# Kernel tuning notes

Hardware: AMD Instinct MI355X
Metric: run time of the kernel (lower is better)

The kernel has to match this reference:

```python
import jax, jax.numpy as jnp
import numpy as np

NEG_SLOPE_GAT = 0.2    # PyG GATConv default negative_slope
NEG_SLOPE_ACT = 0.01   # F.leaky_relu default
D_DIRECTIONS = 4       # len(target): message directions per variable (uniform in this setup)
GAT_HEADS = 4


def gru_cell(x, h, Wih, Whh, bih, bhh):
    # torch.nn.GRUCell math; Wih [3H, in], Whh [3H, H]
    gi = x @ Wih.T + bih
    gh = h @ Whh.T + bhh
    ir, iz, inn = jnp.split(gi, 3, axis=1)
    hr, hz, hn = jnp.split(gh, 3, axis=1)
    r = jax.nn.sigmoid(ir + hr)
    z = jax.nn.sigmoid(iz + hz)
    n = jnp.tanh(inn + r * hn)
    return (1.0 - z) * n + z * h


def gat_conv(x, W, a_src, a_dst, bias, src, dst, heads, concat):
    # PyG GATConv (self-loops already included in src/dst)
    N = x.shape[0]
    C = W.shape[1] // heads
    h = (x @ W).reshape(N, heads, C)
    as_ = jnp.einsum('nhc,hc->nh', h, a_src)
    ad = jnp.einsum('nhc,hc->nh', h, a_dst)
    e = jax.nn.leaky_relu(as_[src] + ad[dst], NEG_SLOPE_GAT)  # [E, heads]
    m = jax.ops.segment_max(e, dst, num_segments=N)
    ex = jnp.exp(e - m[dst])
    den = jax.ops.segment_sum(ex, dst, num_segments=N)
    alpha = ex / den[dst]
    out = jax.ops.segment_sum(h[src] * alpha[:, :, None], dst, num_segments=N)
    if concat:
        return out.reshape(N, heads * C) + bias
    return out.mean(axis=1) + bias


def setup_inputs():
    key = jax.random.key(0)
    ki = iter(jax.random.split(key, 64))
    nk = lambda: next(ki)
    Nx, A, B = 100000, 50000, 50000
    IC, PD = 16, 3
    GH = IC - PD  # gru hidden = 13
    E, M, G, L, H, OC = 2000000, 1024, 1024, 4, 4, 32
    Ntot = Nx + A + B

    def p(*shape):
        return jax.random.normal(nk(), shape, jnp.float32) * 0.05

    inp = {}
    inp['x'] = jax.random.normal(nk(), (Nx, IC), jnp.float32)
    inp['edge_index'] = jax.random.randint(nk(), (2, E), 0, Ntot)
    inp['ass_to_sum_msg'] = jax.random.normal(nk(), (A, 1), jnp.float32)
    inp['ass_to_sum_hidden'] = jax.random.normal(nk(), (A, GH), jnp.float32)
    inp['sum_to_ass_msg'] = jax.random.normal(nk(), (B, 1), jnp.float32)
    inp['sum_to_ass_hidden'] = jax.random.normal(nk(), (B, GH), jnp.float32)
    inp['prefix'] = jax.random.normal(nk(), (A + B, PD), jnp.float32)
    inp['function_node_idxes'] = jax.random.randint(nk(), (M,), 0, Ntot)
    # regularized neighbor_idx_info: group g has direction idx=group_idx[g], src list group_src[g]
    # with idx at position 0 (out_i == 0) and no other entry equal to idx.
    gidx = jax.random.randint(nk(), (G,), 0, M)
    gs = jax.random.randint(nk(), (G, L), 0, M)
    rest = jnp.where(gs[:, 1:] == gidx[:, None], (gidx[:, None] + 1) % M, gs[:, 1:])
    inp['group_idx'] = gidx
    inp['group_src'] = jnp.concatenate([gidx[:, None], rest], axis=1)
    # GRU params
    for g in ('gru1', 'gru2'):
        inp[g + '_Wih'] = p(3 * GH, 1)
        inp[g + '_Whh'] = p(3 * GH, GH)
        inp[g + '_bih'] = p(3 * GH)
        inp[g + '_bhh'] = p(3 * GH)
    # GATConv params (W stored [in, heads*out], used as x @ W)
    inp['W1'] = p(IC, 32); inp['asrc1'] = p(4, 8); inp['adst1'] = p(4, 8); inp['b1'] = p(32)
    inp['W2'] = p(32, 32); inp['asrc2'] = p(4, 8); inp['adst2'] = p(4, 8); inp['b2'] = p(32)
    inp['W3'] = p(32, 32); inp['asrc3'] = p(4, 8); inp['adst3'] = p(4, 8); inp['b3'] = p(32)
    inp['W4'] = p(32, 4 * OC); inp['asrc4'] = p(4, OC); inp['adst4'] = p(4, OC); inp['b4'] = p(OC)
    # Attention heads: Wq/Wk [H, OC, OC] (applied as v @ Wq[h]), Ws [H, 2*OC], bs [H]
    inp['Wq'] = p(H, OC, OC); inp['Wk'] = p(H, OC, OC); inp['Ws'] = p(H, 2 * OC); inp['bs'] = p(H)
    return inp


def reference(x, edge_index, ass_to_sum_msg, ass_to_sum_hidden, sum_to_ass_msg,
              sum_to_ass_hidden, prefix, function_node_idxes, group_idx, group_src,
              gru1_Wih, gru1_Whh, gru1_bih, gru1_bhh,
              gru2_Wih, gru2_Whh, gru2_bih, gru2_bhh,
              W1, asrc1, adst1, b1, W2, asrc2, adst2, b2,
              W3, asrc3, adst3, b3, W4, asrc4, adst4, b4,
              Wq, Wk, Ws, bs):
    h1 = gru_cell(ass_to_sum_msg, ass_to_sum_hidden, gru1_Wih, gru1_Whh, gru1_bih, gru1_bhh)
    h2 = gru_cell(sum_to_ass_msg, sum_to_ass_hidden, gru2_Wih, gru2_Whh, gru2_bih, gru2_bhh)
    hidden = jnp.concatenate([h1, h2], axis=0)
    hidden = jnp.concatenate([prefix, hidden], axis=1)
    xx = jnp.concatenate([x, hidden], axis=0)
    N = xx.shape[0]
    loop = jnp.arange(N)
    src = jnp.concatenate([edge_index[0], loop])  # add self loops (PyG default)
    dst = jnp.concatenate([edge_index[1], loop])
    xx = jax.nn.leaky_relu(gat_conv(xx, W1, asrc1, adst1, b1, src, dst, GAT_HEADS, True), NEG_SLOPE_ACT)
    xx = jax.nn.leaky_relu(gat_conv(xx, W2, asrc2, adst2, b2, src, dst, GAT_HEADS, True), NEG_SLOPE_ACT)
    xx = jax.nn.leaky_relu(gat_conv(xx, W3, asrc3, adst3, b3, src, dst, GAT_HEADS, True), NEG_SLOPE_ACT)
    xx = jax.nn.leaky_relu(gat_conv(xx, W4, asrc4, adst4, b4, src, dst, GAT_HEADS, False), NEG_SLOPE_ACT)
    pooling = xx[function_node_idxes]  # [M, OC]
    hdim = pooling.shape[1]
    # score(i,j,h) = sigmoid((pooling_i @ Wq_h) . ws_q_h + (pooling_j @ Wk_h) . ws_k_h + bs_h)
    # (associativity: equals sigmoid(score_proj(cat([q_proj, k_proj]))) of the original)
    Vq = jnp.einsum('hdo,ho->hd', Wq, Ws[:, :hdim])
    Vk = jnp.einsum('hdo,ho->hd', Wk, Ws[:, hdim:])
    sq = pooling @ Vq.T  # [M, H]
    sk = pooling @ Vk.T  # [M, H]
    scores = jax.nn.sigmoid(sq[:, None, :] + sk[None, :, :] + bs)  # [M, M, H]; flat n -> (n//M, n%M)
    idx = group_idx
    nbr = group_src[:, 1:]  # idx itself sits at position 0 and is removed
    gathered = scores[idx[:, None], nbr]  # [G, L-1, H]
    trg = scores[idx, idx]                # [G, H]
    score_sum = gathered.mean(axis=1)
    tw = jax.nn.softmax(jnp.stack([score_sum, trg], axis=0), axis=0)  # [2, G, H]
    w = jax.nn.softmax(gathered, axis=1) * tw[0][:, None, :] * (D_DIRECTIONS - 1)
    weights = jnp.concatenate([tw[1][:, None, :], w], axis=1)  # [G, L, H] (out_i == 0)
    return weights, h1, h2
```

## Files before the change

kernel.cpp:

```cpp
#include <hip/hip_runtime.h>
#include <hip/hip_bf16.h>

#define NXD   100000
#define AROWS 50000
#define NND   200000
#define EED   2000000
#define ETOT  2200000
#define GHD   13
#define MMD   1024

#define OUT_H1 16384
#define OUT_H2 (16384 + AROWS * GHD)

#define NB    196
#define BSH   10
#define CAP   16000
#define TILE  4096

#define ASM_BLK    7422
#define GRU_BLK    392
#define FEAT_BLK   1563

typedef __hip_bfloat16 bf16;
typedef unsigned int uvec4 __attribute__((ext_vector_type(4)));

__device__ __forceinline__ float bf2f(bf16 v) { return __bfloat162float(v); }
__device__ __forceinline__ float sigm(float x) { return 1.f / (1.f + __expf(-x)); }
__device__ __forceinline__ float tanhfast(float x) {
    x = fminf(15.f, fmaxf(-15.f, x));
    float t = __expf(-2.f * x);
    return (1.f - t) / (1.f + t);
}
__device__ __forceinline__ float lrelu(float x, float s) { return x > 0.f ? x : s * x; }

__device__ __forceinline__ unsigned short f2bf_bits(float v) {
    bf16 b = __float2bfloat16(v);
    return *reinterpret_cast<unsigned short*>(&b);
}
__device__ __forceinline__ float bflo(unsigned int u) { return __uint_as_float((u & 0xFFFFu) << 16); }
__device__ __forceinline__ float bfhi(unsigned int u) { return __uint_as_float(u & 0xFFFF0000u); }

__device__ __forceinline__ float loadF(const void* p, size_t i, int f32) {
    return f32 ? ((const float*)p)[i] : bf2f(((const bf16*)p)[i]);
}
__device__ __forceinline__ void storeF(void* p, size_t i, float v, int f32) {
    if (f32) ((float*)p)[i] = v;
    else ((bf16*)p)[i] = __float2bfloat16(v);
}

__device__ __forceinline__ int flag_from_x(const void* xp, int tid, int* fl) {
    if (tid < 64) {
        const unsigned short* u = (const unsigned short*)xp;
        unsigned short b = u[tid * 2];
        int e = (b >> 7) & 0xFF;
        int viol = (e == 0xFF) || (e < 64) || (e > 190);
        unsigned long long mask = __ballot(viol != 0);
        if (tid == 0) *fl = (__popcll(mask) > 8) ? 1 : 0;
    }
    __syncthreads();
    return *fl;
}

__global__ void bin_kernel(const int* __restrict__ src_e, const int* __restrict__ dst_e,
                           int* __restrict__ gtail, unsigned int* __restrict__ stage) {
    __shared__ int hist[NB];
    __shared__ int base[NB];
    __shared__ int cur[NB];
    int tid = threadIdx.x;
    for (int i = tid; i < NB; i += 256) hist[i] = 0;
    __syncthreads();
    int t0 = blockIdx.x * TILE;
    int tend = t0 + TILE; if (tend > ETOT) tend = ETOT;
    for (int t = t0 + tid; t < tend; t += 256) {
        int d = (t < EED) ? dst_e[t] : (t - EED);
        atomicAdd(&hist[d >> BSH], 1);
    }
    __syncthreads();
    for (int i = tid; i < NB; i += 256) {
        int c = hist[i];
        base[i] = (c > 0) ? atomicAdd(&gtail[i], c) : 0;
        cur[i] = 0;
    }
    __syncthreads();
    for (int t = t0 + tid; t < tend; t += 256) {
        int s, d;
        if (t < EED) { s = src_e[t]; d = dst_e[t]; } else { s = d = t - EED; }
        int b = d >> BSH;
        int p = base[b] + atomicAdd(&cur[b], 1);
        if (p < CAP)
            stage[(size_t)b * CAP + p] = ((unsigned int)(d & 1023) << 18) | (unsigned int)s;
    }
}

__global__ void asmgru_kernel(const void* __restrict__ x, const void* __restrict__ prefix,
                              const void* __restrict__ msg1, const void* __restrict__ hid1,
                              const void* __restrict__ Wih1, const void* __restrict__ Whh1,
                              const void* __restrict__ bih1, const void* __restrict__ bhh1,
                              const void* __restrict__ msg2, const void* __restrict__ hid2,
                              const void* __restrict__ Wih2, const void* __restrict__ Whh2,
                              const void* __restrict__ bih2, const void* __restrict__ bhh2,
                              void* __restrict__ dout, bf16* __restrict__ bufA) {
    __shared__ float WhhL[39 * 13], WihL[39], bihL[39], bhhL[39];
    __shared__ int fl;
    int bid = blockIdx.x, tid = threadIdx.x;
    int f = flag_from_x(x, tid, &fl);
    if (bid < ASM_BLK) {
        int t = bid * 256 + tid;
        if (t < NXD * 16) {
            bufA[t] = __float2bfloat16(loadF(x, t, f));
        } else {
            int u = t - NXD * 16;
            if (u < NXD * 3) {
                int r = u / 3, c = u - r * 3;
                bufA[(size_t)(NXD + r) * 16 + c] = __float2bfloat16(loadF(prefix, u, f));
            }
        }
        return;
    }
    int vb = bid - ASM_BLK;
    int which = vb >= 196;
    const void* msg = which ? msg2 : msg1;
    const void* hid = which ? hid2 : hid1;
    const void* Wih = which ? Wih2 : Wih1;
    const void* Whh = which ? Whh2 : Whh1;
    const void* bih = which ? bih2 : bih1;
    const void* bhh = which ? bhh2 : bhh1;
    size_t houtbase = which ? (size_t)OUT_H2 : (size_t)OUT_H1;
    int rowbase = which ? AROWS : 0;
    int blk = vb - (which ? 196 : 0);
    for (int i = tid; i < 39 * 13; i += 256) WhhL[i] = loadF(Whh, i, f);
    if (tid < 39) { WihL[tid] = loadF(Wih, tid, f); bihL[tid] = loadF(bih, tid, f); bhhL[tid] = loadF(bhh, tid, f); }
    __syncthreads();
    int n = blk * 256 + tid;
    if (n >= AROWS) return;
    float xv = loadF(msg, n, f);
    float h[GHD];
#pragma unroll
    for (int k = 0; k < GHD; k++) h[k] = loadF(hid, n * GHD + k, f);
#pragma unroll
    for (int k = 0; k < GHD; k++) {
        float gir = fmaf(xv, WihL[k],      bihL[k]);
        float giz = fmaf(xv, WihL[13 + k], bihL[13 + k]);
        float gin = fmaf(xv, WihL[26 + k], bihL[26 + k]);
        float ghr = bhhL[k], ghz = bhhL[13 + k], ghn = bhhL[26 + k];
#pragma unroll
        for (int q = 0; q < GHD; q++) {
            ghr = fmaf(h[q], WhhL[k * 13 + q],        ghr);
            ghz = fmaf(h[q], WhhL[(13 + k) * 13 + q], ghz);
            ghn = fmaf(h[q], WhhL[(26 + k) * 13 + q], ghn);
        }
        float r = sigm(gir + ghr);
        float z = sigm(giz + ghz);
        float nn = tanhfast(gin + r * ghn);
        float o = (1.f - z) * nn + z * h[k];
        storeF(dout, houtbase + (size_t)n * GHD + k, o, f);
        bufA[(size_t)(NXD + rowbase + n) * 16 + 3 + k] = __float2bfloat16(o);
    }
}

template <int K>
__device__ __forceinline__ void feat_body(const bf16* __restrict__ xx,
                                          const void* __restrict__ W,
                                          bf16* __restrict__ hbuf, int f,
                                          int vbid, int tid) {
    int j = tid & 31;
    float Wc[K];
#pragma unroll
    for (int k = 0; k < K; k++) Wc[k] = loadF(W, k * 32 + j, f);
    int half = vbid * 8 + (tid >> 5);
    if (half >= NND / 16) return;
    int n0 = half * 16;
#pragma unroll 4
    for (int n = n0; n < n0 + 16; n++) {
        const uvec4* xr4 = (const uvec4*)(xx + (size_t)n * K);
        float v = 0.f;
#pragma unroll
        for (int q = 0; q < K / 8; q++) {
            uvec4 u = xr4[q];
            v = fmaf(bflo(u.x), Wc[q * 8 + 0], v);
            v = fmaf(bfhi(u.x), Wc[q * 8 + 1], v);
            v = fmaf(bflo(u.y), Wc[q * 8 + 2], v);
            v = fmaf(bfhi(u.y), Wc[q * 8 + 3], v);
            v = fmaf(bflo(u.z), Wc[q * 8 + 4], v);
            v = fmaf(bfhi(u.z), Wc[q * 8 + 5], v);
            v = fmaf(bflo(u.w), Wc[q * 8 + 6], v);
            v = fmaf(bfhi(u.w), Wc[q * 8 + 7], v);
        }
        hbuf[(size_t)n * 32 + j] = __float2bfloat16(v);
    }
}

__global__ void mid_kernel(const unsigned int* __restrict__ stage, const int* __restrict__ gtail,
                           int* __restrict__ offs, int* __restrict__ csr,
                           const bf16* __restrict__ xx, const void* __restrict__ W,
                           bf16* __restrict__ hbuf, const void* __restrict__ x) {
    __shared__ int cnt[1024];
    __shared__ int loc[1024];
    __shared__ int cur[1024];
    __shared__ int lds[256];
    __shared__ int fl;
    int bid = blockIdx.x, tid = threadIdx.x;
    if (bid >= NB) {
        int f = flag_from_x(x, tid, &fl);
        feat_body<16>(xx, W, hbuf, f, bid - NB, tid);
        return;
    }
    int b = bid;
    int v = (tid < NB) ? gtail[tid] : 0;
    lds[tid] = v; __syncthreads();
    for (int off = 1; off < 256; off <<= 1) {
        int t2 = (tid >= off) ? lds[tid - off] : 0;
        __syncthreads();
        lds[tid] += t2;
        __syncthreads();
    }
    __shared__ int ebs;
    if (tid == b) ebs = lds[tid] - v;
    __syncthreads();
    int eb = ebs;
    int nE = gtail[b]; if (nE > CAP) nE = CAP;
    const unsigned int* st = stage + (size_t)b * CAP;
    for (int i = tid; i < 1024; i += 256) cnt[i] = 0;
    __syncthreads();
    for (int i = tid; i < nE; i += 256)
        atomicAdd(&cnt[st[i] >> 18], 1);
    __syncthreads();
    int c0 = cnt[tid * 4], c1 = cnt[tid * 4 + 1], c2 = cnt[tid * 4 + 2], c3 = cnt[tid * 4 + 3];
    int s = c0 + c1 + c2 + c3;
    lds[tid] = s; __syncthreads();
    for (int off = 1; off < 256; off <<= 1) {
        int t2 = (tid >= off) ? lds[tid - off] : 0;
        __syncthreads();
        lds[tid] += t2;
        __syncthreads();
    }
    int run = lds[tid] - s;
    loc[tid * 4]     = run;
    loc[tid * 4 + 1] = run + c0;
    loc[tid * 4 + 2] = run + c0 + c1;
    loc[tid * 4 + 3] = run + c0 + c1 + c2;
    __syncthreads();
    int nodebase = b << BSH;
    for (int i = tid; i < 1024; i += 256) {
        cur[i] = loc[i];
        int n = nodebase + i;
        if (n < NND) offs[n] = eb + loc[i];
    }
    if (b == 0 && tid == 0) offs[NND] = ETOT;
    __syncthreads();
    for (int i = tid; i < nE; i += 256) {
        unsigned int e = st[i];
        int dl = e >> 18;
        int src = e & 0x3FFFF;
        int p = atomicAdd(&cur[dl], 1);
        csr[eb + p] = src;
    }
}

template <int K>
__global__ void feat_kernel(const bf16* __restrict__ xx, const void* __restrict__ W,
                            bf16* __restrict__ hbuf, const void* __restrict__ x) {
    __shared__ int fl;
    int tid = threadIdx.x;
    int f = flag_from_x(x, tid, &fl);
    feat_body<K>(xx, W, hbuf, f, blockIdx.x, tid);
}

__global__ void __launch_bounds__(256, 8)
agg_kernel(const bf16* __restrict__ hbuf, const int* __restrict__ offs,
           const int* __restrict__ csr, const void* __restrict__ asrc,
           const void* __restrict__ adst, const void* __restrict__ bias,
           bf16* __restrict__ xxout, const void* __restrict__ x) {
    __shared__ float bl[32], asl[32], adl[32];
    __shared__ int fl;
    int tid = threadIdx.x;
    int f = flag_from_x(x, tid, &fl);
    if (tid < 32) {
        bl[tid]  = loadF(bias, tid, f);
        asl[tid] = loadF(asrc, tid, f);
        adl[tid] = loadF(adst, tid, f);
    }
    __syncthreads();
    int n = blockIdx.x * 64 + (tid >> 2);
    int j = tid & 3;
    int cb = 8 * j;
    float A0 = asl[cb], A1 = asl[cb + 1], A2 = asl[cb + 2], A3 = asl[cb + 3];
    float A4 = asl[cb + 4], A5 = asl[cb + 5], A6 = asl[cb + 6], A7 = asl[cb + 7];
    uvec4 hd = *(const uvec4*)(hbuf + (size_t)n * 32 + cb);
    float adv = bflo(hd.x) * adl[cb]     + bfhi(hd.x) * adl[cb + 1]
              + bflo(hd.y) * adl[cb + 2] + bfhi(hd.y) * adl[cb + 3]
              + bflo(hd.z) * adl[cb + 4] + bfhi(hd.z) * adl[cb + 5]
              + bflo(hd.w) * adl[cb + 6] + bfhi(hd.w) * adl[cb + 7];
    int beg = offs[n], end = offs[n + 1];
    int cnt = end - beg;
    const int* cp = csr + beg;
    uvec4 h0 = *(const uvec4*)(hbuf + (size_t)cp[0] * 32 + cb);
    uvec4 h1 = h0;
    if (cnt > 1) h1 = *(const uvec4*)(hbuf + (size_t)cp[1] * 32 + cb);
    float den = 0.f;
    float a0 = 0.f, a1 = 0.f, a2 = 0.f, a3 = 0.f, a4 = 0.f, a5 = 0.f, a6 = 0.f, a7 = 0.f;
    for (int i = 0; i < cnt; i++) {
        uvec4 hn = (uvec4)(0u);
        if (i + 2 < cnt) {
            int sn = cp[i + 2];
            hn = *(const uvec4*)(hbuf + (size_t)sn * 32 + cb);
        }
        float v0 = bflo(h0.x), v1 = bfhi(h0.x), v2 = bflo(h0.y), v3 = bfhi(h0.y);
        float v4 = bflo(h0.z), v5 = bfhi(h0.z), v6 = bflo(h0.w), v7 = bfhi(h0.w);
        float as = v0 * A0 + v1 * A1 + v2 * A2 + v3 * A3
                 + v4 * A4 + v5 * A5 + v6 * A6 + v7 * A7;
        float e = as + adv;
        e = e > 0.f ? e : 0.2f * e;
        e = fminf(50.f, fmaxf(-50.f, e));
        float w = __expf(e);
        den += w;
        a0 = fmaf(w, v0, a0); a1 = fmaf(w, v1, a1);
        a2 = fmaf(w, v2, a2); a3 = fmaf(w, v3, a3);
        a4 = fmaf(w, v4, a4); a5 = fmaf(w, v5, a5);
        a6 = fmaf(w, v6, a6); a7 = fmaf(w, v7, a7);
        h0 = h1; h1 = hn;
    }
    float inv = 1.f / den;
    float o0 = lrelu(fmaf(a0, inv, bl[cb + 0]), 0.01f);
    float o1 = lrelu(fmaf(a1, inv, bl[cb + 1]), 0.01f);
    float o2 = lrelu(fmaf(a2, inv, bl[cb + 2]), 0.01f);
    float o3 = lrelu(fmaf(a3, inv, bl[cb + 3]), 0.01f);
    float o4 = lrelu(fmaf(a4, inv, bl[cb + 4]), 0.01f);
    float o5 = lrelu(fmaf(a5, inv, bl[cb + 5]), 0.01f);
    float o6 = lrelu(fmaf(a6, inv, bl[cb + 6]), 0.01f);
    float o7 = lrelu(fmaf(a7, inv, bl[cb + 7]), 0.01f);
    uvec4 p;
    p.x = ((unsigned int)f2bf_bits(o1) << 16) | f2bf_bits(o0);
    p.y = ((unsigned int)f2bf_bits(o3) << 16) | f2bf_bits(o2);
    p.z = ((unsigned int)f2bf_bits(o5) << 16) | f2bf_bits(o4);
    p.w = ((unsigned int)f2bf_bits(o7) << 16) | f2bf_bits(o6);
    __builtin_nontemporal_store(p, (uvec4*)(xxout + (size_t)n * 32 + cb));
}

__global__ void layer4_kernel(const bf16* __restrict__ xx,
                              const void* __restrict__ W4,
                              const void* __restrict__ asrc,
                              const void* __restrict__ adst,
                              const void* __restrict__ b4,
                              const int* __restrict__ fidx, const int* __restrict__ offs,
                              const int* __restrict__ csr, float* __restrict__ pool,
                              const void* __restrict__ x) {
    __shared__ float Wl[32 * 128];
    __shared__ float asl[128], adl[128], bl[32];
    __shared__ float accs[4][32];
    __shared__ float dens[4];
    __shared__ int fl;
    int tid = threadIdx.x;
    int f = flag_from_x(x, tid, &fl);
    for (int i = tid; i < 32 * 128; i += 256) Wl[i] = loadF(W4, i, f);
    if (tid < 128) { asl[tid] = loadF(asrc, tid, f); adl[tid] = loadF(adst, tid, f); accs[tid >> 5][tid & 31] = 0.f; }
    if (tid < 32) bl[tid] = loadF(b4, tid, f);
    if (tid < 4) dens[tid] = 0.f;
    __syncthreads();
    int g = blockIdx.x;
    int d = fidx[g];
    int wave = tid >> 6, lane = tid & 63;
    int c = lane & 31;
    int h0 = lane >> 5;
    int h1 = h0 + 2;
    const uvec4* xd4 = (const uvec4*)(xx + (size_t)d * 32);
    uvec4 du0 = xd4[0], du1 = xd4[1];
    float v0 = 0.f, v1 = 0.f;
    {
        unsigned int us[8] = {du0.x, du0.y, du0.z, du0.w, du1.x, du1.y, du1.z, du1.w};
#pragma unroll
        for (int q = 0; q < 8; q++) {
            unsigned int u = us[q];
            int k = 2 * q;
            v0 = fmaf(bflo(u), Wl[k * 128 + lane], v0);       v0 = fmaf(bfhi(u), Wl[(k + 1) * 128 + lane], v0);
            v1 = fmaf(bflo(u), Wl[k * 128 + lane + 64], v1);  v1 = fmaf(bfhi(u), Wl[(k + 1) * 128 + lane + 64], v1);
        }
    }
    float ad0 = v0 * adl[h0 * 32 + c];
    float ad1 = v1 * adl[h1 * 32 + c];
#pragma unroll
    for (int mk = 1; mk < 32; mk <<= 1) { ad0 += __shfl_xor(ad0, mk); ad1 += __shfl_xor(ad1, mk); }
    int beg = offs[d], end = offs[d + 1];
    float den0 = 0.f, den1 = 0.f, acc0 = 0.f, acc1 = 0.f;
    for (int i = beg + wave; i < end; i += 4) {
        int s = csr[i];
        const uvec4* xs4 = (const uvec4*)(xx + (size_t)s * 32);
        uvec4 su0 = xs4[0], su1 = xs4[1];
        float s0 = 0.f, s1 = 0.f;
        unsigned int us[8] = {su0.x, su0.y, su0.z, su0.w, su1.x, su1.y, su1.z, su1.w};
#pragma unroll
        for (int q = 0; q < 8; q++) {
            unsigned int u = us[q];
            int k = 2 * q;
            s0 = fmaf(bflo(u), Wl[k * 128 + lane], s0);       s0 = fmaf(bfhi(u), Wl[(k + 1) * 128 + lane], s0);
            s1 = fmaf(bflo(u), Wl[k * 128 + lane + 64], s1);  s1 = fmaf(bfhi(u), Wl[(k + 1) * 128 + lane + 64], s1);
        }
        float as0 = s0 * asl[h0 * 32 + c];
        float as1 = s1 * asl[h1 * 32 + c];
#pragma unroll
        for (int mk = 1; mk < 32; mk <<= 1) { as0 += __shfl_xor(as0, mk); as1 += __shfl_xor(as1, mk); }
        float e0 = lrelu(as0 + ad0, 0.2f);
        float e1 = lrelu(as1 + ad1, 0.2f);
        e0 = fminf(50.f, fmaxf(-50.f, e0));
        e1 = fminf(50.f, fmaxf(-50.f, e1));
        float w0 = __expf(e0), w1 = __expf(e1);
        den0 += w0; acc0 = fmaf(w0, s0, acc0);
        den1 += w1; acc1 = fmaf(w1, s1, acc1);
    }
    atomicAdd(&accs[h0][c], acc0);
    atomicAdd(&accs[h1][c], acc1);
    if (c == 0) { atomicAdd(&dens[h0], den0); atomicAdd(&dens[h1], den1); }
    __syncthreads();
    if (tid < 32) {
        float t = accs[0][tid] / dens[0] + accs[1][tid] / dens[1]
                + accs[2][tid] / dens[2] + accs[3][tid] / dens[3];
        float o = t * 0.25f + bl[tid];
        pool[g * 32 + tid] = lrelu(o, 0.01f);
    }
}

__global__ void tail_kernel(const void* __restrict__ Wq, const void* __restrict__ Wk,
                            const void* __restrict__ Ws, const void* __restrict__ bs,
                            const int* __restrict__ gidx, const int* __restrict__ gsrc,
                            const float* __restrict__ pool, void* __restrict__ out,
                            const void* __restrict__ x) {
    __shared__ float vq[128], vk[128];
    __shared__ float sq[4096], sk[4096];
    __shared__ int fl;
    int tid = threadIdx.x;
    int f = flag_from_x(x, tid, &fl);
    {
        int which = tid >> 7;
        int i = tid & 127;
        int h = i >> 5, dd = i & 31;
        const void* Wm = which ? Wk : Wq;
        float sum = 0.f;
#pragma unroll
        for (int o = 0; o < 32; o++)
            sum = fmaf(loadF(Wm, (h * 32 + dd) * 32 + o, f), loadF(Ws, h * 64 + which * 32 + o, f), sum);
        (which ? vk : vq)[i] = sum;
    }
    __syncthreads();
    for (int idx = tid; idx < 8192; idx += 256) {
        int which = idx >> 12;
        int i = idx & 4095;
        int g = i >> 2, h = i & 3;
        const float* V = which ? vk : vq;
        float s = 0.f;
#pragma unroll
        for (int dd = 0; dd < 32; dd++) s = fmaf(pool[g * 32 + dd], V[h * 32 + dd], s);
        (which ? sk : sq)[i] = s;
    }
    __syncthreads();
    for (int t = tid; t < 4096; t += 256) {
        int g = t >> 2, h = t & 3;
        int i = gidx[g];
        float bsv = loadF(bs, h, f);
        float sqi = sq[i * 4 + h];
        float trg = sigm(sqi + sk[i * 4 + h] + bsv);
        float ga[3];
#pragma unroll
        for (int q = 0; q < 3; q++) {
            int jj = gsrc[g * 4 + 1 + q];
            ga[q] = sigm(sqi + sk[jj * 4 + h] + bsv);
        }
        float ss = (ga[0] + ga[1] + ga[2]) * (1.f / 3.f);
        float mx = fmaxf(ss, trg);
        float e0 = __expf(ss - mx), e1 = __expf(trg - mx);
        float inv = 1.f / (e0 + e1);
        float tw0 = e0 * inv, tw1 = e1 * inv;
        float mg = fmaxf(ga[0], fmaxf(ga[1], ga[2]));
        float w0 = __expf(ga[0] - mg), w1 = __expf(ga[1] - mg), w2 = __expf(ga[2] - mg);
        float wi = tw0 * 3.f / (w0 + w1 + w2);
        storeF(out, g * 16 + 0 + h,  tw1,     f);
        storeF(out, g * 16 + 4 + h,  w0 * wi, f);
        storeF(out, g * 16 + 8 + h,  w1 * wi, f);
        storeF(out, g * 16 + 12 + h, w2 * wi, f);
    }
}

extern "C" void kernel_launch(void* const* d_in, const int* in_sizes, int n_in,
                              void* d_out, int out_size, void* d_ws, size_t ws_size,
                              hipStream_t stream) {
    const void* x        = d_in[0];
    const int*  ei       = (const int*)d_in[1];
    const void* a2s_msg  = d_in[2];
    const void* a2s_hid  = d_in[3];
    const void* s2a_msg  = d_in[4];
    const void* s2a_hid  = d_in[5];
    const void* prefix   = d_in[6];
    const int*  fidx     = (const int*)d_in[7];
    const int*  gidx     = (const int*)d_in[8];
    const int*  gsrc     = (const int*)d_in[9];
    const void* g1_Wih   = d_in[10];
    const void* g1_Whh   = d_in[11];
    const void* g1_bih   = d_in[12];
    const void* g1_bhh   = d_in[13];
    const void* g2_Wih   = d_in[14];
    const void* g2_Whh   = d_in[15];
    const void* g2_bih   = d_in[16];
    const void* g2_bhh   = d_in[17];
    const void* W1  = d_in[18];
    const void* as1 = d_in[19];
    const void* ad1 = d_in[20];
    const void* b1  = d_in[21];
    const void* W2  = d_in[22];
    const void* as2 = d_in[23];
    const void* ad2 = d_in[24];
    const void* b2  = d_in[25];
    const void* W3  = d_in[26];
    const void* as3 = d_in[27];
    const void* ad3 = d_in[28];
    const void* b3  = d_in[29];
    const void* W4  = d_in[30];
    const void* as4 = d_in[31];
    const void* ad4 = d_in[32];
    const void* b4  = d_in[33];
    const void* Wq  = d_in[34];
    const void* Wk  = d_in[35];
    const void* Ws  = d_in[36];
    const void* bs  = d_in[37];

    const int* src_e = ei;
    const int* dst_e = ei + EED;

    char* wp = (char*)d_ws;
    auto alloc = [&](size_t bytes) {
        char* p = wp;
        wp += (bytes + 255) & ~(size_t)255;
        return p;
    };
    int*   csr   = (int*)alloc((size_t)ETOT * 4);
    int*   offs  = (int*)alloc((size_t)(NND + 1) * 4);
    int*   gtail = (int*)alloc((size_t)NB * 4);
    float* pool  = (float*)alloc((size_t)MMD * 32 * 4);
    bf16*  bufA  = (bf16*)alloc((size_t)NND * 32 * 2);
    bf16*  bufB  = (bf16*)alloc((size_t)NND * 32 * 2);
    unsigned int* stage = (unsigned int*)alloc((size_t)NB * CAP * 4);

    hipMemsetAsync(gtail, 0, (size_t)NB * 4, stream);
    bin_kernel<<<(ETOT + TILE - 1) / TILE, 256, 0, stream>>>(src_e, dst_e, gtail, stage);
    asmgru_kernel<<<ASM_BLK + GRU_BLK, 256, 0, stream>>>(
        x, prefix,
        a2s_msg, a2s_hid, g1_Wih, g1_Whh, g1_bih, g1_bhh,
        s2a_msg, s2a_hid, g2_Wih, g2_Whh, g2_bih, g2_bhh,
        d_out, bufA);

    mid_kernel<<<NB + FEAT_BLK, 256, 0, stream>>>(stage, gtail, offs, csr, bufA, W1, bufB, x);

    const int nblk_agg = NND / 64;
    agg_kernel<<<nblk_agg, 256, 0, stream>>>(bufB, offs, csr, as1, ad1, b1, bufA, x);
    feat_kernel<32><<<FEAT_BLK, 256, 0, stream>>>(bufA, W2, bufB, x);
    agg_kernel<<<nblk_agg, 256, 0, stream>>>(bufB, offs, csr, as2, ad2, b2, bufA, x);
    feat_kernel<32><<<FEAT_BLK, 256, 0, stream>>>(bufA, W3, bufB, x);
    agg_kernel<<<nblk_agg, 256, 0, stream>>>(bufB, offs, csr, as3, ad3, b3, bufA, x);

    layer4_kernel<<<MMD, 256, 0, stream>>>(bufA, W4, as4, ad4, b4, fidx, offs, csr, pool, x);
    tail_kernel<<<1, 256, 0, stream>>>(Wq, Wk, Ws, bs, gidx, gsrc, pool, d_out, x);
}
```

Before: 446.2 us.

## Use per-wave histograms in binning and process eight x elements per thread

The edge binning kernel now keeps a separate shared histogram per wavefront and turns it into per-wave base offsets, which replaces the global-plus-local cursor and lowers contention on shared atomics. The x-to-bf16 conversion in the assemble/GRU kernel now handles eight elements per thread, which cuts that part's block count and flag_from_x overhead; prefix conversion moves to its own block range. The ordering of edges within a bin changes but stays valid. Occupancy in the conversion part is lower, and its loads are still scalar rather than vectorised.

```diff
diff --git a/kernel.cpp b/kernel.cpp
--- a/kernel.cpp
+++ b/kernel.cpp
@@ -17,7 +17,8 @@
 #define CAP   16000
 #define TILE  4096
 
-#define ASM_BLK    7422
+#define X8_BLK     782
+#define PFX_BLK    1172
 #define GRU_BLK    392
 #define FEAT_BLK   1563
 
@@ -63,30 +64,33 @@
 
 __global__ void bin_kernel(const int* __restrict__ src_e, const int* __restrict__ dst_e,
                            int* __restrict__ gtail, unsigned int* __restrict__ stage) {
-    __shared__ int hist[NB];
-    __shared__ int base[NB];
-    __shared__ int cur[NB];
+    __shared__ int whist[4][NB];
     int tid = threadIdx.x;
-    for (int i = tid; i < NB; i += 256) hist[i] = 0;
+    int w = tid >> 6;
+    for (int i = tid; i < 4 * NB; i += 256) ((int*)whist)[i] = 0;
     __syncthreads();
     int t0 = blockIdx.x * TILE;
     int tend = t0 + TILE; if (tend > ETOT) tend = ETOT;
     for (int t = t0 + tid; t < tend; t += 256) {
         int d = (t < EED) ? dst_e[t] : (t - EED);
-        atomicAdd(&hist[d >> BSH], 1);
-    }
-    __syncthreads();
-    for (int i = tid; i < NB; i += 256) {
-        int c = hist[i];
-        base[i] = (c > 0) ? atomicAdd(&gtail[i], c) : 0;
-        cur[i] = 0;
+        atomicAdd(&whist[w][d >> BSH], 1);
+    }
+    __syncthreads();
+    for (int b = tid; b < NB; b += 256) {
+        int c0 = whist[0][b], c1 = whist[1][b], c2 = whist[2][b], c3 = whist[3][b];
+        int tot = c0 + c1 + c2 + c3;
+        int base = tot ? atomicAdd(&gtail[b], tot) : 0;
+        whist[0][b] = base;
+        whist[1][b] = base + c0;
+        whist[2][b] = base + c0 + c1;
+        whist[3][b] = base + c0 + c1 + c2;
     }
     __syncthreads();
     for (int t = t0 + tid; t < tend; t += 256) {
         int s, d;
         if (t < EED) { s = src_e[t]; d = dst_e[t]; } else { s = d = t - EED; }
         int b = d >> BSH;
-        int p = base[b] + atomicAdd(&cur[b], 1);
+        int p = atomicAdd(&whist[w][b], 1);
         if (p < CAP)
             stage[(size_t)b * CAP + p] = ((unsigned int)(d & 1023) << 18) | (unsigned int)s;
     }
@@ -104,20 +108,24 @@
     __shared__ int fl;
     int bid = blockIdx.x, tid = threadIdx.x;
     int f = flag_from_x(x, tid, &fl);
-    if (bid < ASM_BLK) {
-        int t = bid * 256 + tid;
-        if (t < NXD * 16) {
-            bufA[t] = __float2bfloat16(loadF(x, t, f));
-        } else {
-            int u = t - NXD * 16;
-            if (u < NXD * 3) {
-                int r = u / 3, c = u - r * 3;
-                bufA[(size_t)(NXD + r) * 16 + c] = __float2bfloat16(loadF(prefix, u, f));
-            }
+    if (bid < X8_BLK) {
+        int base = bid * 2048 + tid * 8;
+#pragma unroll
+        for (int q = 0; q < 8; q++) {
+            int t = base + q;
+            if (t < NXD * 16) bufA[t] = __float2bfloat16(loadF(x, t, f));
         }
         return;
     }
-    int vb = bid - ASM_BLK;
+    if (bid < X8_BLK + PFX_BLK) {
+        int u = (bid - X8_BLK) * 256 + tid;
+        if (u < NXD * 3) {
+            int r = u / 3, c = u - r * 3;
+            bufA[(size_t)(NXD + r) * 16 + c] = __float2bfloat16(loadF(prefix, u, f));
+        }
+        return;
+    }
+    int vb = bid - X8_BLK - PFX_BLK;
     int which = vb >= 196;
     const void* msg = which ? msg2 : msg1;
     const void* hid = which ? hid2 : hid1;
@@ -540,7 +548,7 @@
 
     hipMemsetAsync(gtail, 0, (size_t)NB * 4, stream);
     bin_kernel<<<(ETOT + TILE - 1) / TILE, 256, 0, stream>>>(src_e, dst_e, gtail, stage);
-    asmgru_kernel<<<ASM_BLK + GRU_BLK, 256, 0, stream>>>(
+    asmgru_kernel<<<X8_BLK + PFX_BLK + GRU_BLK, 256, 0, stream>>>(
         x, prefix,
         a2s_msg, a2s_hid, g1_Wih, g1_Whh, g1_bih, g1_bhh,
         s2a_msg, s2a_hid, g2_Wih, g2_Whh, g2_bih, g2_bhh,
```

Measured after the change: 449.8 us. About the same (+0.8%).
